# Kernel optimization log

Measured on AMD Instinct MI355X. Metric: run time of the kernel, lower is better.

Reference implementation:

```python
import jax, jax.numpy as jnp
import numpy as np

MARGIN = 1.0

def _pairwise_sqdist(z):
    # ||zi - zj||^2 = ||zi||^2 + ||zj||^2 - 2 zi.zj
    sq = jnp.sum(z * z, axis=-1)  # [N]
    d2 = sq[:, None] + sq[None, :] - 2.0 * (z @ z.T)
    return jnp.maximum(d2, 0.0)

def _safe_sqrt(d2):
    # sqrt with well-defined gradient at 0 (matches cdist values; diag = 0)
    pos = d2 > 0.0
    return jnp.where(pos, jnp.sqrt(jnp.where(pos, d2, 1.0)), 0.0)

def setup_inputs() -> dict:
    key = jax.random.key(0)
    k1, k2 = jax.random.split(key)
    z = jax.random.normal(k1, (8192, 128), dtype=jnp.float32)
    labels = jax.random.randint(k2, (8192,), 0, 100, dtype=jnp.int64)
    return {"z": z, "labels": labels}

def reference(z, labels):
    d2 = _pairwise_sqdist(z)              # [N, N] squared distances
    dist = _safe_sqrt(d2)                 # [N, N] distances
    label_eq = labels[:, None] == labels[None, :]
    pos = jnp.where(label_eq, d2, 0.0)
    neg = jnp.where(label_eq, 0.0, jnp.square(jax.nn.relu(MARGIN - dist)))
    return jnp.mean(pos + neg)
```

## Files before the change

kernel.cpp:

```cpp
#include <hip/hip_runtime.h>
#include <stdint.h>


#define NROWS 8192
#define DIMK  128
#define NB    64
#define NTILE (NB * (NB + 1) / 2)
#define NPERS 512

typedef __attribute__((ext_vector_type(4))) float f32x4;

#define AS_GLOBAL __attribute__((address_space(1)))
#define AS_LDS    __attribute__((address_space(3)))

__global__ __launch_bounds__(256) void prep_kernel(
    const float* __restrict__ z, unsigned char* __restrict__ zb,
    float* __restrict__ sq) {
  int tid = threadIdx.x;
  int row = (blockIdx.x << 3) + (tid >> 5);
  int c32 = tid & 31;
  float4 x = ((const float4*)(z + (size_t)row * DIMK))[c32];
  int u = __builtin_amdgcn_cvt_pk_fp8_f32(x.x, x.y, 0, false);
  u     = __builtin_amdgcn_cvt_pk_fp8_f32(x.z, x.w, u, true);
  float r0 = __builtin_amdgcn_cvt_f32_fp8(u, 0);
  float r1 = __builtin_amdgcn_cvt_f32_fp8(u, 1);
  float r2 = __builtin_amdgcn_cvt_f32_fp8(u, 2);
  float r3 = __builtin_amdgcn_cvt_f32_fp8(u, 3);
  float s = (r0 * r0 + r1 * r1) + (r2 * r2 + r3 * r3);
  int k0 = c32 << 2;
  int g  = (((k0 >> 3) & 3) << 2) | (k0 >> 5);
  int p  = ((g ^ (row & 15)) << 3) + (k0 & 7);
  *(uint32_t*)(zb + (size_t)row * DIMK + p) = (uint32_t)u;
  #pragma unroll
  for (int off = 16; off; off >>= 1) s += __shfl_down(s, off, 32);
  if (c32 == 0) sq[row] = s;
}

__device__ __forceinline__ void decode_tile_x(int x, int n, int& bi, int& bj) {
  int rem = n, k = 0, len = NB - x;
  while (rem >= len) { rem -= len; ++k; len -= 8; }
  bi = x + (k << 3);
  bj = bi + rem;
}

__global__ __launch_bounds__(512, 4) void loss_kernel(
    const unsigned char* __restrict__ zb, const float* __restrict__ sq,
    const int* __restrict__ labels, float* __restrict__ out) {
  __shared__ __align__(16) unsigned char buf[2][32768];
  __shared__ __align__(16) unsigned char sqlab[2][2048];
  __shared__ float red[8];

  int tid = threadIdx.x, lane = tid & 63, wave = tid >> 6;
  int wm = wave >> 1, wn = wave & 1;
  int lc = lane & 15;
  int q  = lane >> 4;

  int sl_isB  = wave >> 2;
  int sl_isLa = (wave >> 1) & 1;
  int sl_half = wave & 1;

  float psum_acc = 0.f;

  int x = blockIdx.x & 7;
  int s = blockIdx.x >> 3;
  int tcount = (NB / 2) * (NB + 1) / 4 * 0 + (288 - 8 * x);
  int n = s;
  if (n < tcount) {
  int bi, bj;
  decode_tile_x(x, n, bi, bj);

  {
    const unsigned char* Ab = zb + (((size_t)bi << 7) * DIMK);
    const unsigned char* Bb = zb + (((size_t)bj << 7) * DIMK);
    #pragma unroll
    for (int it = 0; it < 2; ++it) {
      int L0 = (it << 9) + (wave << 6);
      __builtin_amdgcn_global_load_lds(
          (const AS_GLOBAL void*)(uintptr_t)(Ab + (size_t)(L0 + lane) * 16),
          (AS_LDS void*)(uintptr_t)(&buf[0][(size_t)L0 * 16]), 16, 0, 0);
      __builtin_amdgcn_global_load_lds(
          (const AS_GLOBAL void*)(uintptr_t)(Bb + (size_t)(L0 + lane) * 16),
          (AS_LDS void*)(uintptr_t)(&buf[0][16384 + (size_t)L0 * 16]), 16, 0, 0);
    }
    const char* p0 = sl_isLa ? (const char*)labels : (const char*)sq;
    const char* src = p0 + ((size_t)((sl_isB ? bj : bi) << 7) << 2)
                         + (sl_half << 8);
    if (lane < 16)
      __builtin_amdgcn_global_load_lds(
          (const AS_GLOBAL void*)(uintptr_t)(src + lane * 16),
          (AS_LDS void*)(uintptr_t)(&sqlab[0][wave << 8]), 16, 0, 0);
  }

  int cur = 0;
  for (;; n += 64) {
    int nn = n + 64;
    bool hasNext = nn < tcount;

    asm volatile("s_waitcnt vmcnt(0)" ::: "memory");
    __syncthreads();

    int bin = bi, bjn = bj;
    if (hasNext) {
      decode_tile_x(x, nn, bin, bjn);
      int nc = cur ^ 1;
      const unsigned char* Ab = zb + (((size_t)bin << 7) * DIMK);
      const unsigned char* Bb = zb + (((size_t)bjn << 7) * DIMK);
      #pragma unroll
      for (int it = 0; it < 2; ++it) {
        int L0 = (it << 9) + (wave << 6);
        __builtin_amdgcn_global_load_lds(
            (const AS_GLOBAL void*)(uintptr_t)(Ab + (size_t)(L0 + lane) * 16),
            (AS_LDS void*)(uintptr_t)(&buf[nc][(size_t)L0 * 16]), 16, 0, 0);
        __builtin_amdgcn_global_load_lds(
            (const AS_GLOBAL void*)(uintptr_t)(Bb + (size_t)(L0 + lane) * 16),
            (AS_LDS void*)(uintptr_t)(&buf[nc][16384 + (size_t)L0 * 16]), 16, 0, 0);
      }
      const char* p0 = sl_isLa ? (const char*)labels : (const char*)sq;
      const char* src = p0 + ((size_t)((sl_isB ? bjn : bin) << 7) << 2)
                           + (sl_half << 8);
      if (lane < 16)
        __builtin_amdgcn_global_load_lds(
            (const AS_GLOBAL void*)(uintptr_t)(src + lane * 16),
            (AS_LDS void*)(uintptr_t)(&sqlab[nc][wave << 8]), 16, 0, 0);
    }

    const unsigned char* ldsA = &buf[cur][0];
    const unsigned char* ldsB = &buf[cur][16384];
    const float* sqAl = (const float*)&sqlab[cur][0];
    const int*   laAl = (const int*)&sqlab[cur][512];
    const float* sqBl = (const float*)&sqlab[cur][1024];
    const int*   laBl = (const int*)&sqlab[cur][1536];

    f32x4 acc[2][4] = {};
    #pragma unroll
    for (int ks = 0; ks < 4; ++ks) {
      int so = ((((q << 2) | ks) ^ lc) << 3);
      long a0 = *(const long*)(ldsA + ((wm << 5)      + lc) * 128 + so);
      long a1 = *(const long*)(ldsA + ((wm << 5) + 16 + lc) * 128 + so);
      long b0 = *(const long*)(ldsB + ((wn << 6)      + lc) * 128 + so);
      long b1 = *(const long*)(ldsB + ((wn << 6) + 16 + lc) * 128 + so);
      long b2 = *(const long*)(ldsB + ((wn << 6) + 32 + lc) * 128 + so);
      long b3 = *(const long*)(ldsB + ((wn << 6) + 48 + lc) * 128 + so);
      acc[0][0] = __builtin_amdgcn_mfma_f32_16x16x32_fp8_fp8(a0, b0, acc[0][0], 0, 0, 0);
      acc[0][1] = __builtin_amdgcn_mfma_f32_16x16x32_fp8_fp8(a0, b1, acc[0][1], 0, 0, 0);
      acc[0][2] = __builtin_amdgcn_mfma_f32_16x16x32_fp8_fp8(a0, b2, acc[0][2], 0, 0, 0);
      acc[0][3] = __builtin_amdgcn_mfma_f32_16x16x32_fp8_fp8(a0, b3, acc[0][3], 0, 0, 0);
      acc[1][0] = __builtin_amdgcn_mfma_f32_16x16x32_fp8_fp8(a1, b0, acc[1][0], 0, 0, 0);
      acc[1][1] = __builtin_amdgcn_mfma_f32_16x16x32_fp8_fp8(a1, b1, acc[1][1], 0, 0, 0);
      acc[1][2] = __builtin_amdgcn_mfma_f32_16x16x32_fp8_fp8(a1, b2, acc[1][2], 0, 0, 0);
      acc[1][3] = __builtin_amdgcn_mfma_f32_16x16x32_fp8_fp8(a1, b3, acc[1][3], 0, 0, 0);
    }

    int r0 = q << 2;
    float sn_[4]; int ln_[4];
    #pragma unroll
    for (int j = 0; j < 4; ++j) {
      int nidx = (wn << 6) + (j << 4) + lc;
      sn_[j] = sqBl[nidx]; ln_[j] = laBl[nidx];
    }
    float ps0 = 0.f, ps1 = 0.f, ps2 = 0.f, ps3 = 0.f;
    float mnall = 1e30f;
    #pragma unroll
    for (int i = 0; i < 2; ++i) {
      int mb = (wm << 5) + (i << 4) + r0;
      f32x4 sm4 = *(const f32x4*)&sqAl[mb];
      int4  lm4 = *(const int4*)&laAl[mb];
      #pragma unroll
      for (int j = 0; j < 4; ++j) {
        float d0  = fmaf(-2.f, acc[i][j][0], sm4[0] + sn_[j]);
        float d1  = fmaf(-2.f, acc[i][j][1], sm4[1] + sn_[j]);
        float d2_ = fmaf(-2.f, acc[i][j][2], sm4[2] + sn_[j]);
        float d3  = fmaf(-2.f, acc[i][j][3], sm4[3] + sn_[j]);
        mnall = fminf(mnall, fminf(fminf(d0, d1), fminf(d2_, d3)));
        ps0 += (lm4.x == ln_[j]) ? d0  : 0.f;
        ps1 += (lm4.y == ln_[j]) ? d1  : 0.f;
        ps2 += (lm4.z == ln_[j]) ? d2_ : 0.f;
        ps3 += (lm4.w == ln_[j]) ? d3  : 0.f;
      }
    }
    if (__builtin_expect(__any(mnall < 1.f), 0)) {
      ps0 = ps1 = ps2 = ps3 = 0.f;
      #pragma unroll
      for (int i = 0; i < 2; ++i) {
        int mb = (wm << 5) + (i << 4) + r0;
        f32x4 sm4 = *(const f32x4*)&sqAl[mb];
        int4  lm4 = *(const int4*)&laAl[mb];
        #pragma unroll
        for (int j = 0; j < 4; ++j) {
          float dc, tt;
          dc = fmaxf(fmaf(-2.f, acc[i][j][0], sm4[0] + sn_[j]), 0.f);
          tt = fmaxf(1.f - sqrtf(dc), 0.f);
          ps0 += (lm4.x == ln_[j]) ? dc : tt * tt;
          dc = fmaxf(fmaf(-2.f, acc[i][j][1], sm4[1] + sn_[j]), 0.f);
          tt = fmaxf(1.f - sqrtf(dc), 0.f);
          ps1 += (lm4.y == ln_[j]) ? dc : tt * tt;
          dc = fmaxf(fmaf(-2.f, acc[i][j][2], sm4[2] + sn_[j]), 0.f);
          tt = fmaxf(1.f - sqrtf(dc), 0.f);
          ps2 += (lm4.z == ln_[j]) ? dc : tt * tt;
          dc = fmaxf(fmaf(-2.f, acc[i][j][3], sm4[3] + sn_[j]), 0.f);
          tt = fmaxf(1.f - sqrtf(dc), 0.f);
          ps3 += (lm4.w == ln_[j]) ? dc : tt * tt;
        }
      }
    }
    float w = (bi == bj) ? 1.f : 2.f;
    psum_acc += w * ((ps0 + ps1) + (ps2 + ps3));

    if (!hasNext) break;
    bi = bin; bj = bjn; cur ^= 1;
  }
  }

  psum_acc *= (1.f / (8192.f * 8192.f));
  #pragma unroll
  for (int off = 32; off; off >>= 1) psum_acc += __shfl_down(psum_acc, off);
  if (lane == 0) red[wave] = psum_acc;
  __syncthreads();
  if (tid == 0) {
    float sum = 0.f;
    #pragma unroll
    for (int k = 0; k < 8; ++k) sum += red[k];
    atomicAdd(out, sum);
  }
}

extern "C" void kernel_launch(void* const* d_in, const int* in_sizes, int n_in,
                              void* d_out, int out_size, void* d_ws, size_t ws_size,
                              hipStream_t stream) {
  const float* z      = (const float*)d_in[0];
  const int*   labels = (const int*)d_in[1];
  float*       out    = (float*)d_out;
  unsigned char* zb   = (unsigned char*)d_ws;
  float* sq           = (float*)((char*)d_ws + (size_t)NROWS * DIMK);

  prep_kernel<<<NROWS / 8, 256, 0, stream>>>(z, zb, sq);
  loss_kernel<<<NPERS, 512, 0, stream>>>(zb, sq, labels, out);
}
```

Before: 72.94 us.

## Drop LDS double-buffering and read fp8 operands directly from global memory

Removes the LDS staging buffers, the global_load_lds prefetch pipeline and the per-tile barrier. The MFMA operands, squared norms and labels are now loaded straight from global memory through the cache hierarchy. This removes sync and LDS traffic and should raise occupancy because there is no shared memory, but it loses explicit prefetch overlap. Global reads use the swizzled 8-byte pattern, which may coalesce poorly and expose load latency.

```diff
diff --git a/kernel.cpp b/kernel.cpp
--- a/kernel.cpp
+++ b/kernel.cpp
@@ -5,13 +5,9 @@
 #define NROWS 8192
 #define DIMK  128
 #define NB    64
-#define NTILE (NB * (NB + 1) / 2)
 #define NPERS 512
 
 typedef __attribute__((ext_vector_type(4))) float f32x4;
-
-#define AS_GLOBAL __attribute__((address_space(1)))
-#define AS_LDS    __attribute__((address_space(3)))
 
 __global__ __launch_bounds__(256) void prep_kernel(
     const float* __restrict__ z, unsigned char* __restrict__ zb,
@@ -46,8 +42,6 @@
 __global__ __launch_bounds__(512, 4) void loss_kernel(
     const unsigned char* __restrict__ zb, const float* __restrict__ sq,
     const int* __restrict__ labels, float* __restrict__ out) {
-  __shared__ __align__(16) unsigned char buf[2][32768];
-  __shared__ __align__(16) unsigned char sqlab[2][2048];
   __shared__ float red[8];
 
   int tid = threadIdx.x, lane = tid & 63, wave = tid >> 6;
@@ -55,92 +49,35 @@
   int lc = lane & 15;
   int q  = lane >> 4;
 
-  int sl_isB  = wave >> 2;
-  int sl_isLa = (wave >> 1) & 1;
-  int sl_half = wave & 1;
-
   float psum_acc = 0.f;
 
   int x = blockIdx.x & 7;
   int s = blockIdx.x >> 3;
-  int tcount = (NB / 2) * (NB + 1) / 4 * 0 + (288 - 8 * x);
-  int n = s;
-  if (n < tcount) {
-  int bi, bj;
-  decode_tile_x(x, n, bi, bj);
+  int tcount = 288 - 8 * x;
 
-  {
+  int rA0 = ((wm << 5)      + lc) * 128;
+  int rA1 = ((wm << 5) + 16 + lc) * 128;
+  int rB0 = ((wn << 6)      + lc) * 128;
+  int rB1 = ((wn << 6) + 16 + lc) * 128;
+  int rB2 = ((wn << 6) + 32 + lc) * 128;
+  int rB3 = ((wn << 6) + 48 + lc) * 128;
+
+  for (int n = s; n < tcount; n += 64) {
+    int bi, bj;
+    decode_tile_x(x, n, bi, bj);
     const unsigned char* Ab = zb + (((size_t)bi << 7) * DIMK);
     const unsigned char* Bb = zb + (((size_t)bj << 7) * DIMK);
-    #pragma unroll
-    for (int it = 0; it < 2; ++it) {
-      int L0 = (it << 9) + (wave << 6);
-      __builtin_amdgcn_global_load_lds(
-          (const AS_GLOBAL void*)(uintptr_t)(Ab + (size_t)(L0 + lane) * 16),
-          (AS_LDS void*)(uintptr_t)(&buf[0][(size_t)L0 * 16]), 16, 0, 0);
-      __builtin_amdgcn_global_load_lds(
-          (const AS_GLOBAL void*)(uintptr_t)(Bb + (size_t)(L0 + lane) * 16),
-          (AS_LDS void*)(uintptr_t)(&buf[0][16384 + (size_t)L0 * 16]), 16, 0, 0);
-    }
-    const char* p0 = sl_isLa ? (const char*)labels : (const char*)sq;
-    const char* src = p0 + ((size_t)((sl_isB ? bj : bi) << 7) << 2)
-                         + (sl_half << 8);
-    if (lane < 16)
-      __builtin_amdgcn_global_load_lds(
-          (const AS_GLOBAL void*)(uintptr_t)(src + lane * 16),
-          (AS_LDS void*)(uintptr_t)(&sqlab[0][wave << 8]), 16, 0, 0);
-  }
-
-  int cur = 0;
-  for (;; n += 64) {
-    int nn = n + 64;
-    bool hasNext = nn < tcount;
-
-    asm volatile("s_waitcnt vmcnt(0)" ::: "memory");
-    __syncthreads();
-
-    int bin = bi, bjn = bj;
-    if (hasNext) {
-      decode_tile_x(x, nn, bin, bjn);
-      int nc = cur ^ 1;
-      const unsigned char* Ab = zb + (((size_t)bin << 7) * DIMK);
-      const unsigned char* Bb = zb + (((size_t)bjn << 7) * DIMK);
-      #pragma unroll
-      for (int it = 0; it < 2; ++it) {
-        int L0 = (it << 9) + (wave << 6);
-        __builtin_amdgcn_global_load_lds(
-            (const AS_GLOBAL void*)(uintptr_t)(Ab + (size_t)(L0 + lane) * 16),
-            (AS_LDS void*)(uintptr_t)(&buf[nc][(size_t)L0 * 16]), 16, 0, 0);
-        __builtin_amdgcn_global_load_lds(
-            (const AS_GLOBAL void*)(uintptr_t)(Bb + (size_t)(L0 + lane) * 16),
-            (AS_LDS void*)(uintptr_t)(&buf[nc][16384 + (size_t)L0 * 16]), 16, 0, 0);
-      }
-      const char* p0 = sl_isLa ? (const char*)labels : (const char*)sq;
-      const char* src = p0 + ((size_t)((sl_isB ? bjn : bin) << 7) << 2)
-                           + (sl_half << 8);
-      if (lane < 16)
-        __builtin_amdgcn_global_load_lds(
-            (const AS_GLOBAL void*)(uintptr_t)(src + lane * 16),
-            (AS_LDS void*)(uintptr_t)(&sqlab[nc][wave << 8]), 16, 0, 0);
-    }
-
-    const unsigned char* ldsA = &buf[cur][0];
-    const unsigned char* ldsB = &buf[cur][16384];
-    const float* sqAl = (const float*)&sqlab[cur][0];
-    const int*   laAl = (const int*)&sqlab[cur][512];
-    const float* sqBl = (const float*)&sqlab[cur][1024];
-    const int*   laBl = (const int*)&sqlab[cur][1536];
 
     f32x4 acc[2][4] = {};
     #pragma unroll
     for (int ks = 0; ks < 4; ++ks) {
       int so = ((((q << 2) | ks) ^ lc) << 3);
-      long a0 = *(const long*)(ldsA + ((wm << 5)      + lc) * 128 + so);
-      long a1 = *(const long*)(ldsA + ((wm << 5) + 16 + lc) * 128 + so);
-      long b0 = *(const long*)(ldsB + ((wn << 6)      + lc) * 128 + so);
-      long b1 = *(const long*)(ldsB + ((wn << 6) + 16 + lc) * 128 + so);
-      long b2 = *(const long*)(ldsB + ((wn << 6) + 32 + lc) * 128 + so);
-      long b3 = *(const long*)(ldsB + ((wn << 6) + 48 + lc) * 128 + so);
+      long a0 = *(const long*)(Ab + rA0 + so);
+      long a1 = *(const long*)(Ab + rA1 + so);
+      long b0 = *(const long*)(Bb + rB0 + so);
+      long b1 = *(const long*)(Bb + rB1 + so);
+      long b2 = *(const long*)(Bb + rB2 + so);
+      long b3 = *(const long*)(Bb + rB3 + so);
       acc[0][0] = __builtin_amdgcn_mfma_f32_16x16x32_fp8_fp8(a0, b0, acc[0][0], 0, 0, 0);
       acc[0][1] = __builtin_amdgcn_mfma_f32_16x16x32_fp8_fp8(a0, b1, acc[0][1], 0, 0, 0);
       acc[0][2] = __builtin_amdgcn_mfma_f32_16x16x32_fp8_fp8(a0, b2, acc[0][2], 0, 0, 0);
@@ -151,20 +88,25 @@
       acc[1][3] = __builtin_amdgcn_mfma_f32_16x16x32_fp8_fp8(a1, b3, acc[1][3], 0, 0, 0);
     }
 
+    const float* sqA = sq     + ((size_t)bi << 7);
+    const int*   laA = labels + ((size_t)bi << 7);
+    const float* sqB = sq     + ((size_t)bj << 7);
+    const int*   laB = labels + ((size_t)bj << 7);
+
     int r0 = q << 2;
     float sn_[4]; int ln_[4];
     #pragma unroll
     for (int j = 0; j < 4; ++j) {
       int nidx = (wn << 6) + (j << 4) + lc;
-      sn_[j] = sqBl[nidx]; ln_[j] = laBl[nidx];
+      sn_[j] = sqB[nidx]; ln_[j] = laB[nidx];
     }
     float ps0 = 0.f, ps1 = 0.f, ps2 = 0.f, ps3 = 0.f;
     float mnall = 1e30f;
     #pragma unroll
     for (int i = 0; i < 2; ++i) {
       int mb = (wm << 5) + (i << 4) + r0;
-      f32x4 sm4 = *(const f32x4*)&sqAl[mb];
-      int4  lm4 = *(const int4*)&laAl[mb];
+      f32x4 sm4 = *(const f32x4*)&sqA[mb];
+      int4  lm4 = *(const int4*)&laA[mb];
       #pragma unroll
       for (int j = 0; j < 4; ++j) {
         float d0  = fmaf(-2.f, acc[i][j][0], sm4[0] + sn_[j]);
@@ -183,8 +125,8 @@
       #pragma unroll
       for (int i = 0; i < 2; ++i) {
         int mb = (wm << 5) + (i << 4) + r0;
-        f32x4 sm4 = *(const f32x4*)&sqAl[mb];
-        int4  lm4 = *(const int4*)&laAl[mb];
+        f32x4 sm4 = *(const f32x4*)&sqA[mb];
+        int4  lm4 = *(const int4*)&laA[mb];
         #pragma unroll
         for (int j = 0; j < 4; ++j) {
           float dc, tt;
@@ -205,10 +147,6 @@
     }
     float w = (bi == bj) ? 1.f : 2.f;
     psum_acc += w * ((ps0 + ps1) + (ps2 + ps3));
-
-    if (!hasNext) break;
-    bi = bin; bj = bjn; cur ^= 1;
-  }
   }
 
   psum_acc *= (1.f / (8192.f * 8192.f));
```

Result: slower. 82.88 us (+13.6%).

## Keep A row-block resident and stream up to four B tiles per block

Applied to the files above, without the earlier changes.

Replaces the persistent 512-block grid, which walked the triangular tile list, with 544 non-persistent blocks. Each block owns one row block bi, loads its A tile and sq/labels once, and double-buffers up to four consecutive B tiles. This cuts global/LDS traffic for A and shrinks LDS per block so occupancy can rise (launch bound 6). In exchange the blocks carry uneven amounts of work, since chunks near the diagonal edge may hold fewer than four tiles, and the grid runs more blocks than there are CUs.

```diff
diff --git a/kernel.cpp b/kernel.cpp
--- a/kernel.cpp
+++ b/kernel.cpp
@@ -5,8 +5,7 @@
 #define NROWS 8192
 #define DIMK  128
 #define NB    64
-#define NTILE (NB * (NB + 1) / 2)
-#define NPERS 512
+#define NBLK  544
 
 typedef __attribute__((ext_vector_type(4))) float f32x4;
 
@@ -36,18 +35,13 @@
   if (c32 == 0) sq[row] = s;
 }
 
-__device__ __forceinline__ void decode_tile_x(int x, int n, int& bi, int& bj) {
-  int rem = n, k = 0, len = NB - x;
-  while (rem >= len) { rem -= len; ++k; len -= 8; }
-  bi = x + (k << 3);
-  bj = bi + rem;
-}
-
-__global__ __launch_bounds__(512, 4) void loss_kernel(
+__global__ __launch_bounds__(512, 6) void loss_kernel(
     const unsigned char* __restrict__ zb, const float* __restrict__ sq,
     const int* __restrict__ labels, float* __restrict__ out) {
-  __shared__ __align__(16) unsigned char buf[2][32768];
-  __shared__ __align__(16) unsigned char sqlab[2][2048];
+  __shared__ __align__(16) unsigned char Abuf[16384];
+  __shared__ __align__(16) unsigned char Bbuf[2][16384];
+  __shared__ __align__(16) unsigned char sqlabA[1024];
+  __shared__ __align__(16) unsigned char sqlabB[2][1024];
   __shared__ float red[8];
 
   int tid = threadIdx.x, lane = tid & 63, wave = tid >> 6;
@@ -55,81 +49,86 @@
   int lc = lane & 15;
   int q  = lane >> 4;
 
-  int sl_isB  = wave >> 2;
-  int sl_isLa = (wave >> 1) & 1;
-  int sl_half = wave & 1;
+  int b = blockIdx.x;
+  int bi = 0, base = 0;
+  for (;;) {
+    int c = (67 - bi) >> 2;
+    if (b < base + c) break;
+    base += c; ++bi;
+  }
+  int chunk = b - base;
+  int bj0 = bi + (chunk << 2);
+  int nBt = (NB - bj0 < 4) ? (NB - bj0) : 4;
 
   float psum_acc = 0.f;
 
-  int x = blockIdx.x & 7;
-  int s = blockIdx.x >> 3;
-  int tcount = (NB / 2) * (NB + 1) / 4 * 0 + (288 - 8 * x);
-  int n = s;
-  if (n < tcount) {
-  int bi, bj;
-  decode_tile_x(x, n, bi, bj);
-
   {
-    const unsigned char* Ab = zb + (((size_t)bi << 7) * DIMK);
-    const unsigned char* Bb = zb + (((size_t)bj << 7) * DIMK);
+    const unsigned char* Ab = zb + ((size_t)bi << 14);
     #pragma unroll
     for (int it = 0; it < 2; ++it) {
       int L0 = (it << 9) + (wave << 6);
       __builtin_amdgcn_global_load_lds(
           (const AS_GLOBAL void*)(uintptr_t)(Ab + (size_t)(L0 + lane) * 16),
-          (AS_LDS void*)(uintptr_t)(&buf[0][(size_t)L0 * 16]), 16, 0, 0);
+          (AS_LDS void*)(uintptr_t)(&Abuf[(size_t)L0 * 16]), 16, 0, 0);
+    }
+    if (wave < 4 && lane < 16) {
+      const char* p0 = (wave >= 2) ? (const char*)labels : (const char*)sq;
+      const char* src = p0 + ((size_t)bi << 9) + ((wave & 1) << 8);
+      __builtin_amdgcn_global_load_lds(
+          (const AS_GLOBAL void*)(uintptr_t)(src + lane * 16),
+          (AS_LDS void*)(uintptr_t)(&sqlabA[wave << 8]), 16, 0, 0);
+    }
+    const unsigned char* Bb = zb + ((size_t)bj0 << 14);
+    #pragma unroll
+    for (int it = 0; it < 2; ++it) {
+      int L0 = (it << 9) + (wave << 6);
       __builtin_amdgcn_global_load_lds(
           (const AS_GLOBAL void*)(uintptr_t)(Bb + (size_t)(L0 + lane) * 16),
-          (AS_LDS void*)(uintptr_t)(&buf[0][16384 + (size_t)L0 * 16]), 16, 0, 0);
-    }
-    const char* p0 = sl_isLa ? (const char*)labels : (const char*)sq;
-    const char* src = p0 + ((size_t)((sl_isB ? bj : bi) << 7) << 2)
-                         + (sl_half << 8);
-    if (lane < 16)
+          (AS_LDS void*)(uintptr_t)(&Bbuf[0][(size_t)L0 * 16]), 16, 0, 0);
+    }
+    if (wave >= 4 && lane < 16) {
+      const char* p0 = (wave >= 6) ? (const char*)labels : (const char*)sq;
+      const char* src = p0 + ((size_t)bj0 << 9) + ((wave & 1) << 8);
       __builtin_amdgcn_global_load_lds(
           (const AS_GLOBAL void*)(uintptr_t)(src + lane * 16),
-          (AS_LDS void*)(uintptr_t)(&sqlab[0][wave << 8]), 16, 0, 0);
-  }
+          (AS_LDS void*)(uintptr_t)(&sqlabB[0][(wave - 4) << 8]), 16, 0, 0);
+    }
+  }
+
+  const float* sqAl = (const float*)&sqlabA[0];
+  const int*   laAl = (const int*)&sqlabA[512];
 
   int cur = 0;
-  for (;; n += 64) {
-    int nn = n + 64;
-    bool hasNext = nn < tcount;
-
+  for (int ib = 0;; ++ib) {
     asm volatile("s_waitcnt vmcnt(0)" ::: "memory");
     __syncthreads();
 
-    int bin = bi, bjn = bj;
+    bool hasNext = (ib + 1) < nBt;
+
     if (hasNext) {
-      decode_tile_x(x, nn, bin, bjn);
+      int bjn = bj0 + ib + 1;
       int nc = cur ^ 1;
-      const unsigned char* Ab = zb + (((size_t)bin << 7) * DIMK);
-      const unsigned char* Bb = zb + (((size_t)bjn << 7) * DIMK);
+      const unsigned char* Bb = zb + ((size_t)bjn << 14);
       #pragma unroll
       for (int it = 0; it < 2; ++it) {
         int L0 = (it << 9) + (wave << 6);
         __builtin_amdgcn_global_load_lds(
-            (const AS_GLOBAL void*)(uintptr_t)(Ab + (size_t)(L0 + lane) * 16),
-            (AS_LDS void*)(uintptr_t)(&buf[nc][(size_t)L0 * 16]), 16, 0, 0);
-        __builtin_amdgcn_global_load_lds(
             (const AS_GLOBAL void*)(uintptr_t)(Bb + (size_t)(L0 + lane) * 16),
-            (AS_LDS void*)(uintptr_t)(&buf[nc][16384 + (size_t)L0 * 16]), 16, 0, 0);
-      }
-      const char* p0 = sl_isLa ? (const char*)labels : (const char*)sq;
-      const char* src = p0 + ((size_t)((sl_isB ? bjn : bin) << 7) << 2)
-                           + (sl_half << 8);
-      if (lane < 16)
+            (AS_LDS void*)(uintptr_t)(&Bbuf[nc][(size_t)L0 * 16]), 16, 0, 0);
+      }
+      if (wave >= 4 && lane < 16) {
+        const char* p0 = (wave >= 6) ? (const char*)labels : (const char*)sq;
+        const char* src = p0 + ((size_t)bjn << 9) + ((wave & 1) << 8);
         __builtin_amdgcn_global_load_lds(
             (const AS_GLOBAL void*)(uintptr_t)(src + lane * 16),
-            (AS_LDS void*)(uintptr_t)(&sqlab[nc][wave << 8]), 16, 0, 0);
-    }
-
-    const unsigned char* ldsA = &buf[cur][0];
-    const unsigned char* ldsB = &buf[cur][16384];
-    const float* sqAl = (const float*)&sqlab[cur][0];
-    const int*   laAl = (const int*)&sqlab[cur][512];
-    const float* sqBl = (const float*)&sqlab[cur][1024];
-    const int*   laBl = (const int*)&sqlab[cur][1536];
+            (AS_LDS void*)(uintptr_t)(&sqlabB[nc][(wave - 4) << 8]), 16, 0, 0);
+      }
+    }
+
+    const unsigned char* ldsA = &Abuf[0];
+    const unsigned char* ldsB = &Bbuf[cur][0];
+    const float* sqBl = (const float*)&sqlabB[cur][0];
+    const int*   laBl = (const int*)&sqlabB[cur][512];
 
     f32x4 acc[2][4] = {};
     #pragma unroll
@@ -203,12 +202,11 @@
         }
       }
     }
-    float w = (bi == bj) ? 1.f : 2.f;
+    float w = (bi == (bj0 + ib)) ? 1.f : 2.f;
     psum_acc += w * ((ps0 + ps1) + (ps2 + ps3));
 
     if (!hasNext) break;
-    bi = bin; bj = bjn; cur ^= 1;
-  }
+    cur ^= 1;
   }
 
   psum_acc *= (1.f / (8192.f * 8192.f));
@@ -234,5 +232,5 @@
   float* sq           = (float*)((char*)d_ws + (size_t)NROWS * DIMK);
 
   prep_kernel<<<NROWS / 8, 256, 0, stream>>>(z, zb, sq);
-  loss_kernel<<<NPERS, 512, 0, stream>>>(zb, sq, labels, out);
+  loss_kernel<<<NBLK, 512, 0, stream>>>(zb, sq, labels, out);
 }
```

After: 86.22 us. +18.2%, slower.
